# Kernel optimization log

Hardware: AMD Instinct MI355X
Metric: run time of the kernel (lower is better)

## Reference

```python
import jax, jax.numpy as jnp
import numpy as np
import math

B, S, HID, NH = 2, 2048, 1024, 16
HD = HID // NH  # head_dim = 64
TEMPERATURE = 1.0


def setup_inputs() -> dict:
    key = jax.random.key(0)
    ks = jax.random.split(key, 6)
    w = lambda k: (jax.random.normal(k, (HID, HID), dtype=jnp.float32) * 0.02)
    return {
        "hidden_states": jax.random.normal(ks[0], (B, S, HID), dtype=jnp.float32),
        "attention_mask": jnp.ones((B, S), dtype=jnp.float32),
        "Wq": w(ks[1]), "bq": jnp.zeros((HID,), jnp.float32),
        "Wk": w(ks[2]), "bk": jnp.zeros((HID,), jnp.float32),
        "Wv": w(ks[3]), "bv": jnp.zeros((HID,), jnp.float32),
        "Wo": w(ks[4]), "bo": jnp.zeros((HID,), jnp.float32),
    }


def reference(hidden_states, attention_mask, Wq, bq, Wk, bk, Wv, bv, Wo, bo):
    b, s, hid = hidden_states.shape
    heads = lambda x: x.reshape(b, s, NH, HD).transpose(0, 2, 1, 3)  # [b,h,s,d]

    q = heads(hidden_states @ Wq.T + bq)
    k = heads(hidden_states @ Wk.T + bk)
    v = heads(hidden_states @ Wv.T + bv)

    # padding mask applied multiplicatively to k and v
    m = attention_mask[:, None, :, None]  # [b,1,s,1]
    k = k * m
    v = v * m

    # auxiliary Hopfield state: k^T @ v per head -> [b,h,d,d]
    state = jnp.einsum("bhsd,bhse->bhde", k, v)

    # energy / scores
    energy = jnp.einsum("bhqd,bhkd->bhqk", q, k) / (TEMPERATURE * math.sqrt(HD))
    causal = jnp.triu(jnp.ones((s, s), dtype=bool), k=1)  # True above diagonal
    energy = jnp.where(causal[None, None], -jnp.inf, energy)
    energy = jnp.where(attention_mask[:, None, None, :] == 0, -jnp.inf, energy)

    attn = jax.nn.softmax(energy, axis=-1)
    out = jnp.einsum("bhqk,bhkd->bhqd", attn, v)
    out = out.transpose(0, 2, 1, 3).reshape(b, s, hid)
    out = out @ Wo.T + bo
    return out, state
```

## Files before the change

### kernel.cpp

```cpp
#include <hip/hip_runtime.h>
#include <hip/hip_bf16.h>

#define B_ 2
#define S_ 2048
#define HID_ 1024
#define NH_ 16
#define HD_ 64
#define MTOK (B_*S_)
#define LDQKV 3072

typedef __attribute__((ext_vector_type(8))) __bf16 bf16x8;
typedef __attribute__((ext_vector_type(4))) __bf16 bf16x4;
typedef __attribute__((ext_vector_type(4))) float f32x4;

__device__ __forceinline__ void gl16(__bf16* lds, const __bf16* g) {
  __builtin_amdgcn_global_load_lds(
      (const __attribute__((address_space(1))) void*)g,
      (__attribute__((address_space(3))) void*)lds, 16, 0, 0);
}

__global__ __launch_bounds__(256) void cast_all(
    const float* __restrict__ X,
    const float* __restrict__ Wq, const float* __restrict__ Wk,
    const float* __restrict__ Wv, const float* __restrict__ Wo,
    __bf16* __restrict__ Xb, __bf16* __restrict__ Wqkvb, __bf16* __restrict__ Wob)
{
  int i = blockIdx.x * 256 + threadIdx.x;
  const float* src; __bf16* dst; int j;
  if (i < (1 << 20))              { src = X;  dst = Xb;                 j = i; }
  else if (i < (1<<20)+(1<<18))   { src = Wq; dst = Wqkvb;              j = i - (1<<20); }
  else if (i < (1<<20)+(2<<18))   { src = Wk; dst = Wqkvb + (1<<20);    j = i - (1<<20) - (1<<18); }
  else if (i < (1<<20)+(3<<18))   { src = Wv; dst = Wqkvb + (2<<20);    j = i - (1<<20) - (2<<18); }
  else                            { src = Wo; dst = Wob;                j = i - (1<<20) - (3<<18); }
  float4 v = reinterpret_cast<const float4*>(src)[j];
  bf16x4 o;
  o[0] = (__bf16)v.x; o[1] = (__bf16)v.y; o[2] = (__bf16)v.z; o[3] = (__bf16)v.w;
  reinterpret_cast<bf16x4*>(dst)[j] = o;
}

__global__ __launch_bounds__(256) void gemm_qkv(
    const __bf16* __restrict__ A, const __bf16* __restrict__ W,
    const float* __restrict__ bq, const float* __restrict__ bk,
    const float* __restrict__ bv, const float* __restrict__ mask,
    __bf16* __restrict__ C)
{
  __shared__ __bf16 As[2][128 * 32];
  __shared__ __bf16 Bs[2][128 * 32];
  const int t = threadIdx.x;
  const int m0 = blockIdx.y * 128;
  const int n0 = blockIdx.x * 128;
  const int lane = t & 63;
  const int w = t >> 6;
  const int wr = (w >> 1) * 64;
  const int wc = (w & 1) * 64;
  const int fr = lane & 15;
  const int kg = lane >> 4;

  f32x4 acc[4][4];
  #pragma unroll
  for (int i = 0; i < 4; i++)
    #pragma unroll
    for (int j = 0; j < 4; j++) acc[i][j] = (f32x4)0.f;

  const int srow = w * 16 + (lane >> 2);
  const int scol = (lane & 3) * 8;
  const __bf16* ap0 = A + (size_t)(m0 + srow) * HID_ + scol;
  const __bf16* ap1 = A + (size_t)(m0 + 64 + srow) * HID_ + scol;
  const __bf16* wp0 = W + (size_t)(n0 + srow) * HID_ + scol;
  const __bf16* wp1 = W + (size_t)(n0 + 64 + srow) * HID_ + scol;

  #define GSTAGE(buf, koff) \
    gl16(&As[buf][w * 512], ap0 + (koff)); \
    gl16(&As[buf][2048 + w * 512], ap1 + (koff)); \
    gl16(&Bs[buf][w * 512], wp0 + (koff)); \
    gl16(&Bs[buf][2048 + w * 512], wp1 + (koff));

  GSTAGE(0, 0);
  for (int k0 = 0; k0 < HID_; k0 += 32) {
    const int cur = (k0 >> 5) & 1;
    if (k0 + 32 < HID_) {
      GSTAGE(cur ^ 1, k0 + 32);
      asm volatile("s_waitcnt vmcnt(4)" ::: "memory");
    } else {
      asm volatile("s_waitcnt vmcnt(0)" ::: "memory");
    }
    __builtin_amdgcn_sched_barrier(0);
    __builtin_amdgcn_s_barrier();
    bf16x8 af[4], bf[4];
    #pragma unroll
    for (int m = 0; m < 4; m++) af[m] = *(const bf16x8*)&As[cur][(wr + m*16 + fr) * 32 + kg*8];
    #pragma unroll
    for (int n = 0; n < 4; n++) bf[n] = *(const bf16x8*)&Bs[cur][(wc + n*16 + fr) * 32 + kg*8];
    #pragma unroll
    for (int m = 0; m < 4; m++)
      #pragma unroll
      for (int n = 0; n < 4; n++)
        acc[m][n] = __builtin_amdgcn_mfma_f32_16x16x32_bf16(af[m], bf[n], acc[m][n], 0, 0, 0);
    __builtin_amdgcn_s_barrier();
  }

  const int region = n0 >> 10;
  const float* bias = region == 0 ? bq : (region == 1 ? bk : bv);
  const int nloc = n0 & 1023;

  #pragma unroll
  for (int m = 0; m < 4; m++) {
    #pragma unroll
    for (int r = 0; r < 4; r++) {
      int row = m0 + wr + m*16 + kg*4 + r;
      float rs = region ? mask[row] : 1.f;
      #pragma unroll
      for (int n = 0; n < 4; n++) {
        int c = wc + n*16 + fr;
        float v = (acc[m][n][r] + bias[nloc + c]) * rs;
        C[(size_t)row * LDQKV + n0 + c] = (__bf16)v;
      }
    }
  }
}

__global__ __launch_bounds__(256) void gemm_o(
    const __bf16* __restrict__ A, const __bf16* __restrict__ W,
    const float* __restrict__ bias, float* __restrict__ C)
{
  __shared__ __bf16 As[2][128 * 32];
  __shared__ __bf16 Bs[2][128 * 32];
  const int t = threadIdx.x;
  const int m0 = blockIdx.y * 128;
  const int n0 = blockIdx.x * 128;
  const int lane = t & 63;
  const int w = t >> 6;
  const int wr = (w >> 1) * 64;
  const int wc = (w & 1) * 64;
  const int fr = lane & 15;
  const int kg = lane >> 4;

  f32x4 acc[4][4];
  #pragma unroll
  for (int i = 0; i < 4; i++)
    #pragma unroll
    for (int j = 0; j < 4; j++) acc[i][j] = (f32x4)0.f;

  const int srow = w * 16 + (lane >> 2);
  const int scol = (lane & 3) * 8;
  const __bf16* ap0 = A + (size_t)(m0 + srow) * HID_ + scol;
  const __bf16* ap1 = A + (size_t)(m0 + 64 + srow) * HID_ + scol;
  const __bf16* wp0 = W + (size_t)(n0 + srow) * HID_ + scol;
  const __bf16* wp1 = W + (size_t)(n0 + 64 + srow) * HID_ + scol;

  GSTAGE(0, 0);
  for (int k0 = 0; k0 < HID_; k0 += 32) {
    const int cur = (k0 >> 5) & 1;
    if (k0 + 32 < HID_) {
      GSTAGE(cur ^ 1, k0 + 32);
      asm volatile("s_waitcnt vmcnt(4)" ::: "memory");
    } else {
      asm volatile("s_waitcnt vmcnt(0)" ::: "memory");
    }
    __builtin_amdgcn_sched_barrier(0);
    __builtin_amdgcn_s_barrier();
    bf16x8 af[4], bf[4];
    #pragma unroll
    for (int m = 0; m < 4; m++) af[m] = *(const bf16x8*)&As[cur][(wr + m*16 + fr) * 32 + kg*8];
    #pragma unroll
    for (int n = 0; n < 4; n++) bf[n] = *(const bf16x8*)&Bs[cur][(wc + n*16 + fr) * 32 + kg*8];
    #pragma unroll
    for (int m = 0; m < 4; m++)
      #pragma unroll
      for (int n = 0; n < 4; n++)
        acc[m][n] = __builtin_amdgcn_mfma_f32_16x16x32_bf16(af[m], bf[n], acc[m][n], 0, 0, 0);
    __builtin_amdgcn_s_barrier();
  }

  #pragma unroll
  for (int m = 0; m < 4; m++) {
    #pragma unroll
    for (int r = 0; r < 4; r++) {
      int row = m0 + wr + m*16 + kg*4 + r;
      #pragma unroll
      for (int n = 0; n < 4; n++) {
        int col = n0 + wc + n*16 + fr;
        C[(size_t)row * HID_ + col] = acc[m][n][r] + bias[col];
      }
    }
  }
}

__global__ __launch_bounds__(256) void transpose_kv(
    const __bf16* __restrict__ Kin, const __bf16* __restrict__ Vin,
    __bf16* __restrict__ Kt, __bf16* __restrict__ Vt)
{
  __shared__ __bf16 tile[64][68];
  const int tok0 = blockIdx.x * 64;
  const int f0 = blockIdx.y * 64;
  const __bf16* in = blockIdx.z ? Vin : Kin;
  __bf16* out = blockIdx.z ? Vt : Kt;
  const int t = threadIdx.x;
  const int r = t >> 2;
  const int c0 = (t & 3) * 16;
  const __bf16* src = in + (size_t)(tok0 + r) * LDQKV + f0 + c0;
  *(bf16x8*)&tile[r][c0]     = *(const bf16x8*)src;
  *(bf16x8*)&tile[r][c0 + 8] = *(const bf16x8*)(src + 8);
  __syncthreads();
  bf16x8 o0, o1;
  #pragma unroll
  for (int j = 0; j < 8; j++) { o0[j] = tile[c0 + j][r]; o1[j] = tile[c0 + 8 + j][r]; }
  __bf16* dst = out + (size_t)(f0 + r) * MTOK + tok0 + c0;
  *(bf16x8*)dst = o0;
  *(bf16x8*)(dst + 8) = o1;
}

#define SCALE_LOG2E 0.18033688011112043f

__device__ __forceinline__ bf16x8 ld_swz(const __bf16* base, int row, int xb) {
  return *(const bf16x8*)((const char*)base + row * 128 + (xb ^ ((row & 7) << 4)));
}
__device__ __forceinline__ void st_swz16(__bf16* base, int row, int colbyte, __bf16 v) {
  *(__bf16*)((char*)base + row * 128 + (colbyte ^ ((row & 7) << 4))) = v;
}
__device__ __forceinline__ bf16x8 ld_swz256(const __bf16* base, int row, int xb) {
  return *(const bf16x8*)((const char*)base + row * 256 + (xb ^ ((row & 7) << 4)));
}

__device__ __forceinline__ void attn_tile(
    const __bf16* __restrict__ ks, const __bf16* __restrict__ vs,
    const bool (&okm)[4], __bf16* __restrict__ pw,
    const bf16x8 (&qa)[2], f32x4 (&acc)[4], f32x4& accl,
    const bf16x8 ones, int q0w, int kt, int fc, int kg)
{
  f32x4 s[4];
  #pragma unroll
  for (int n = 0; n < 4; n++) s[n] = (f32x4)0.f;
  #pragma unroll
  for (int kd = 0; kd < 2; kd++)
    #pragma unroll
    for (int n = 0; n < 4; n++) {
      bf16x8 kf = ld_swz(ks, n * 16 + fc, kd * 64 + kg * 16);
      s[n] = __builtin_amdgcn_mfma_f32_16x16x32_bf16(qa[kd], kf, s[n], 0, 0, 0);
    }

  const int g4 = kg * 4;
  const bool fullt = (kt * 64 + 63 <= q0w);
  if (fullt) {
    #pragma unroll
    for (int r = 0; r < 4; r++)
      #pragma unroll
      for (int n = 0; n < 4; n++) {
        float p = okm[n] ? __builtin_amdgcn_exp2f(s[n][r] * SCALE_LOG2E) : 0.f;
        st_swz16(pw, g4 + r, (n * 16 + fc) * 2, (__bf16)p);
      }
  } else {
    #pragma unroll
    for (int r = 0; r < 4; r++) {
      const int qg = q0w + g4 + r;
      #pragma unroll
      for (int n = 0; n < 4; n++) {
        bool ok = okm[n] && (kt * 64 + n * 16 + fc <= qg);
        float p = ok ? __builtin_amdgcn_exp2f(s[n][r] * SCALE_LOG2E) : 0.f;
        st_swz16(pw, g4 + r, (n * 16 + fc) * 2, (__bf16)p);
      }
    }
  }

  #pragma unroll
  for (int kc = 0; kc < 2; kc++) {
    bf16x8 pf = ld_swz(pw, fc, kc * 64 + kg * 16);
    accl = __builtin_amdgcn_mfma_f32_16x16x32_bf16(pf, ones, accl, 0, 0, 0);
    #pragma unroll
    for (int n = 0; n < 4; n++) {
      bf16x8 vf = ld_swz(vs, n * 16 + fc, kc * 64 + kg * 16);
      acc[n] = __builtin_amdgcn_mfma_f32_16x16x32_bf16(pf, vf, acc[n], 0, 0, 0);
    }
  }
}

__global__ __launch_bounds__(256) void flash_mfma(
    const __bf16* __restrict__ Q, const __bf16* __restrict__ K,
    const __bf16* __restrict__ Vt, const float* __restrict__ mask,
    __bf16* __restrict__ O)
{
  __shared__ __bf16 Ks[2][64 * 64];
  __shared__ __bf16 Vs[2][64 * 64];
  __shared__ __bf16 Ps[4][16 * 64];

  const int bh = blockIdx.x;
  const int qt = 31 - (int)blockIdx.y;
  const int b = bh >> 4, h = bh & 15;
  const int t = threadIdx.x;
  const int w = t >> 6;
  const int lane = t & 63;
  const int fc = lane & 15;
  const int kg = lane >> 4;
  const int g4 = kg * 4;

  const int q0w = qt * 64 + w * 16;
  const size_t tokbase = (size_t)b * S_;

  const int rr = lane >> 3;
  const int cswz = ((lane & 7) ^ rr) * 8;
  const int ktmax = qt;

  bf16x8 qa[2];
  {
    const __bf16* qp = Q + (tokbase + q0w + fc) * LDQKV + h * HD_;
    qa[0] = *(const bf16x8*)(qp + kg * 8);
    qa[1] = *(const bf16x8*)(qp + 32 + kg * 8);
  }

  const float* mp = mask + tokbase + fc;
  float mnxt[4];
  #pragma unroll
  for (int n = 0; n < 4; n++) mnxt[n] = mp[n * 16];

  const __bf16* kp0 = K + (tokbase + (size_t)(w * 16 + rr)) * LDQKV + h * HD_ + cswz;
  const __bf16* kp1 = kp0 + (size_t)8 * LDQKV;
  const __bf16* vp0 = Vt + (size_t)(h * HD_ + w * 16 + rr) * MTOK + tokbase + cswz;
  const __bf16* vp1 = vp0 + (size_t)8 * MTOK;

  gl16(&Ks[0][(w * 16) * 64],     kp0);
  gl16(&Ks[0][(w * 16 + 8) * 64], kp1);
  gl16(&Vs[0][(w * 16) * 64],     vp0);
  gl16(&Vs[0][(w * 16 + 8) * 64], vp1);
  kp0 += (size_t)64 * LDQKV; kp1 += (size_t)64 * LDQKV;
  vp0 += 64; vp1 += 64;

  bf16x8 ones;
  #pragma unroll
  for (int j = 0; j < 8; j++) ones[j] = (__bf16)1.f;

  f32x4 acc[4], accl;
  #pragma unroll
  for (int n = 0; n < 4; n++) acc[n] = (f32x4)0.f;
  accl = (f32x4)0.f;

  __bf16* pw = &Ps[w][0];

  for (int kt = 0; kt <= ktmax; ++kt) {
    const int cur = kt & 1;
    float mcur[4];
    #pragma unroll
    for (int n = 0; n < 4; n++) mcur[n] = mnxt[n];

    if (kt < ktmax) {
      #pragma unroll
      for (int n = 0; n < 4; n++) mnxt[n] = mp[(kt + 1) * 64 + n * 16];
      const int nxt = cur ^ 1;
      gl16(&Ks[nxt][(w * 16) * 64],     kp0);
      gl16(&Ks[nxt][(w * 16 + 8) * 64], kp1);
      gl16(&Vs[nxt][(w * 16) * 64],     vp0);
      gl16(&Vs[nxt][(w * 16 + 8) * 64], vp1);
      kp0 += (size_t)64 * LDQKV; kp1 += (size_t)64 * LDQKV;
      vp0 += 64; vp1 += 64;
      asm volatile("s_waitcnt vmcnt(8)" ::: "memory");
    } else {
      asm volatile("s_waitcnt vmcnt(0)" ::: "memory");
    }
    __builtin_amdgcn_sched_barrier(0);
    __builtin_amdgcn_s_barrier();

    bool okm[4];
    #pragma unroll
    for (int n = 0; n < 4; n++) okm[n] = (mcur[n] != 0.f);

    attn_tile(&Ks[cur][0], &Vs[cur][0], okm, pw, qa, acc, accl, ones, q0w, kt, fc, kg);

    __builtin_amdgcn_s_barrier();
  }

  #pragma unroll
  for (int r = 0; r < 4; r++) {
    float inv = accl[r] > 0.f ? 1.f / accl[r] : 0.f;
    __bf16* op = O + (tokbase + q0w + g4 + r) * HID_ + h * HD_;
    #pragma unroll
    for (int n = 0; n < 4; n++)
      op[n * 16 + fc] = (__bf16)(acc[n][r] * inv);
  }
}

__global__ __launch_bounds__(256) void state_mfma(
    const __bf16* __restrict__ Kt, const __bf16* __restrict__ Vt,
    float* __restrict__ part)
{
  __shared__ __bf16 Kl[64 * 128];
  __shared__ __bf16 Vl[64 * 128];
  const int bh = blockIdx.x, sc = blockIdx.y;
  const int b = bh >> 4, h = bh & 15;
  const int t = threadIdx.x;
  const int w = t >> 6;
  const int lane = t & 63;
  const int fc = lane & 15;
  const int kg = lane >> 4;
  const size_t colbase = (size_t)b * S_ + sc * 128;
  const int rloc = lane >> 4;
  const int cb = (lane & 15) * 16;

  #pragma unroll
  for (int c = 0; c < 4; c++) {
    int row = w * 16 + c * 4 + rloc;
    int scol = (cb ^ ((row & 7) << 4)) >> 1;
    gl16(&Kl[(w * 16 + c * 4) * 128], Kt + (size_t)(h * HD_ + row) * MTOK + colbase + scol);
    gl16(&Vl[(w * 16 + c * 4) * 128], Vt + (size_t)(h * HD_ + row) * MTOK + colbase + scol);
  }
  __syncthreads();

  f32x4 acc[4];
  #pragma unroll
  for (int n = 0; n < 4; n++) acc[n] = (f32x4)0.f;
  #pragma unroll
  for (int ks = 0; ks < 4; ks++) {
    bf16x8 af = ld_swz256(Kl, w * 16 + fc, ks * 64 + kg * 16);
    #pragma unroll
    for (int n = 0; n < 4; n++) {
      bf16x8 bfr = ld_swz256(Vl, n * 16 + fc, ks * 64 + kg * 16);
      acc[n] = __builtin_amdgcn_mfma_f32_16x16x32_bf16(af, bfr, acc[n], 0, 0, 0);
    }
  }

  float* dst = part + (((size_t)bh * 16 + sc) << 12);
  #pragma unroll
  for (int n = 0; n < 4; n++)
    #pragma unroll
    for (int r = 0; r < 4; r++)
      dst[(w * 16 + kg * 4 + r) * 64 + n * 16 + fc] = acc[n][r];
}

__global__ __launch_bounds__(256) void state_reduce(
    const float* __restrict__ part, float* __restrict__ out)
{
  int i = blockIdx.x * 256 + threadIdx.x;
  int bh = i >> 12, de = i & 4095;
  float s = 0.f;
  #pragma unroll
  for (int sc = 0; sc < 16; sc++) s += part[(((size_t)bh * 16 + sc) << 12) + de];
  out[i] = s;
}

extern "C" void kernel_launch(void* const* d_in, const int* in_sizes, int n_in,
                              void* d_out, int out_size, void* d_ws, size_t ws_size,
                              hipStream_t stream)
{
  const float* hs   = (const float*)d_in[0];
  const float* mask = (const float*)d_in[1];
  const float* Wq   = (const float*)d_in[2];
  const float* bq   = (const float*)d_in[3];
  const float* Wk   = (const float*)d_in[4];
  const float* bk   = (const float*)d_in[5];
  const float* Wv   = (const float*)d_in[6];
  const float* bv   = (const float*)d_in[7];
  const float* Wo   = (const float*)d_in[8];
  const float* bo   = (const float*)d_in[9];
  float* out = (float*)d_out;

  char* ws = (char*)d_ws;
  __bf16* Wqkvb = (__bf16*)(ws);
  __bf16* Wob   = (__bf16*)(ws + (6u  << 20));
  __bf16* Xb    = (__bf16*)(ws + (8u  << 20));
  __bf16* QKV   = (__bf16*)(ws + (16u << 20));
  __bf16* Ob    = (__bf16*)(ws + (40u << 20));
  __bf16* Ktg   = (__bf16*)(ws + (48u << 20));

  cast_all<<<8192, 256, 0, stream>>>(hs, Wq, Wk, Wv, Wo, Xb, Wqkvb, Wob);

  gemm_qkv<<<dim3(LDQKV / 128, MTOK / 128), 256, 0, stream>>>(
      Xb, Wqkvb, bq, bk, bv, mask, QKV);

  __bf16* Vtg = Xb;
  transpose_kv<<<dim3(MTOK / 64, HID_ / 64, 2), 256, 0, stream>>>(
      QKV + 1024, QKV + 2048, Ktg, Vtg);

  flash_mfma<<<dim3(B_ * NH_, 32), 256, 0, stream>>>(
      QKV, QKV + 1024, Vtg, mask, Ob);

  gemm_o<<<dim3(HID_ / 128, MTOK / 128), 256, 0, stream>>>(Ob, Wob, bo, out);

  float* part = (float*)Ob;
  state_mfma<<<dim3(B_ * NH_, 16), 256, 0, stream>>>(Ktg, Vtg, part);
  state_reduce<<<512, 256, 0, stream>>>(part, out + (size_t)MTOK * HID_);
}
```

Baseline: 136.0 us.

## Triple-buffer GEMM pipeline with swizzled LDS, fuse state reduce into gemm_o

After: 126.3 us. -7.1%, faster.

```diff
diff --git a/kernel.cpp b/kernel.cpp
--- a/kernel.cpp
+++ b/kernel.cpp
@@ -18,6 +18,8 @@
       (const __attribute__((address_space(1))) void*)g,
       (__attribute__((address_space(3))) void*)lds, 16, 0, 0);
 }
+
+__device__ __forceinline__ int gswz(int row) { return ((row ^ (row >> 2)) & 3) << 4; }
 
 __global__ __launch_bounds__(256) void cast_all(
     const float* __restrict__ X,
@@ -44,8 +46,7 @@
     const float* __restrict__ bv, const float* __restrict__ mask,
     __bf16* __restrict__ C)
 {
-  __shared__ __bf16 As[2][128 * 32];
-  __shared__ __bf16 Bs[2][128 * 32];
+  __shared__ __bf16 SM[24576];
   const int t = threadIdx.x;
   const int m0 = blockIdx.y * 128;
   const int n0 = blockIdx.x * 128;
@@ -63,40 +64,51 @@
     for (int j = 0; j < 4; j++) acc[i][j] = (f32x4)0.f;
 
   const int srow = w * 16 + (lane >> 2);
-  const int scol = (lane & 3) * 8;
-  const __bf16* ap0 = A + (size_t)(m0 + srow) * HID_ + scol;
-  const __bf16* ap1 = A + (size_t)(m0 + 64 + srow) * HID_ + scol;
-  const __bf16* wp0 = W + (size_t)(n0 + srow) * HID_ + scol;
-  const __bf16* wp1 = W + (size_t)(n0 + 64 + srow) * HID_ + scol;
-
-  #define GSTAGE(buf, koff) \
-    gl16(&As[buf][w * 512], ap0 + (koff)); \
-    gl16(&As[buf][2048 + w * 512], ap1 + (koff)); \
-    gl16(&Bs[buf][w * 512], wp0 + (koff)); \
-    gl16(&Bs[buf][2048 + w * 512], wp1 + (koff));
-
-  GSTAGE(0, 0);
-  for (int k0 = 0; k0 < HID_; k0 += 32) {
-    const int cur = (k0 >> 5) & 1;
-    if (k0 + 32 < HID_) {
-      GSTAGE(cur ^ 1, k0 + 32);
-      asm volatile("s_waitcnt vmcnt(4)" ::: "memory");
-    } else {
-      asm volatile("s_waitcnt vmcnt(0)" ::: "memory");
-    }
+  const int scolb = ((lane & 3) * 16) ^ gswz(srow);
+  const __bf16* ap0 = A + (size_t)(m0 + srow) * HID_ + (scolb >> 1);
+  const __bf16* ap1 = A + (size_t)(m0 + 64 + srow) * HID_ + (scolb >> 1);
+  const __bf16* wp0 = W + (size_t)(n0 + srow) * HID_ + (scolb >> 1);
+  const __bf16* wp1 = W + (size_t)(n0 + 64 + srow) * HID_ + (scolb >> 1);
+
+  #define STAGE3(buf, koff) { \
+    __bf16* ab = SM + (buf) * 4096; \
+    __bf16* bb = SM + 12288 + (buf) * 4096; \
+    gl16(ab + w * 512, ap0 + (koff)); \
+    gl16(ab + 2048 + w * 512, ap1 + (koff)); \
+    gl16(bb + w * 512, wp0 + (koff)); \
+    gl16(bb + 2048 + w * 512, wp1 + (koff)); }
+
+  STAGE3(0, 0);
+  STAGE3(1, 32);
+  int bc = 0, bp2 = 2;
+  for (int step = 0; step < 32; ++step) {
+    if (step + 1 < 32) { asm volatile("s_waitcnt vmcnt(4)" ::: "memory"); }
+    else               { asm volatile("s_waitcnt vmcnt(0)" ::: "memory"); }
     __builtin_amdgcn_sched_barrier(0);
     __builtin_amdgcn_s_barrier();
+    if (step + 2 < 32) STAGE3(bp2, (step + 2) * 32);
+
+    const __bf16* ab = SM + bc * 4096;
+    const __bf16* bb = SM + 12288 + bc * 4096;
     bf16x8 af[4], bf[4];
     #pragma unroll
-    for (int m = 0; m < 4; m++) af[m] = *(const bf16x8*)&As[cur][(wr + m*16 + fr) * 32 + kg*8];
-    #pragma unroll
-    for (int n = 0; n < 4; n++) bf[n] = *(const bf16x8*)&Bs[cur][(wc + n*16 + fr) * 32 + kg*8];
+    for (int m = 0; m < 4; m++) {
+      int row = wr + m*16 + fr;
+      af[m] = *(const bf16x8*)((const char*)ab + row * 64 + ((kg * 16) ^ gswz(row)));
+    }
+    #pragma unroll
+    for (int n = 0; n < 4; n++) {
+      int row = wc + n*16 + fr;
+      bf[n] = *(const bf16x8*)((const char*)bb + row * 64 + ((kg * 16) ^ gswz(row)));
+    }
     #pragma unroll
     for (int m = 0; m < 4; m++)
       #pragma unroll
       for (int n = 0; n < 4; n++)
         acc[m][n] = __builtin_amdgcn_mfma_f32_16x16x32_bf16(af[m], bf[n], acc[m][n], 0, 0, 0);
-    __builtin_amdgcn_s_barrier();
+
+    bc = (bc == 2) ? 0 : bc + 1;
+    bp2 = (bp2 == 2) ? 0 : bp2 + 1;
   }
 
   const int region = n0 >> 10;
@@ -112,75 +124,7 @@
       #pragma unroll
       for (int n = 0; n < 4; n++) {
         int c = wc + n*16 + fr;
-        float v = (acc[m][n][r] + bias[nloc + c]) * rs;
-        C[(size_t)row * LDQKV + n0 + c] = (__bf16)v;
-      }
-    }
-  }
-}
-
-__global__ __launch_bounds__(256) void gemm_o(
-    const __bf16* __restrict__ A, const __bf16* __restrict__ W,
-    const float* __restrict__ bias, float* __restrict__ C)
-{
-  __shared__ __bf16 As[2][128 * 32];
-  __shared__ __bf16 Bs[2][128 * 32];
-  const int t = threadIdx.x;
-  const int m0 = blockIdx.y * 128;
-  const int n0 = blockIdx.x * 128;
-  const int lane = t & 63;
-  const int w = t >> 6;
-  const int wr = (w >> 1) * 64;
-  const int wc = (w & 1) * 64;
-  const int fr = lane & 15;
-  const int kg = lane >> 4;
-
-  f32x4 acc[4][4];
-  #pragma unroll
-  for (int i = 0; i < 4; i++)
-    #pragma unroll
-    for (int j = 0; j < 4; j++) acc[i][j] = (f32x4)0.f;
-
-  const int srow = w * 16 + (lane >> 2);
-  const int scol = (lane & 3) * 8;
-  const __bf16* ap0 = A + (size_t)(m0 + srow) * HID_ + scol;
-  const __bf16* ap1 = A + (size_t)(m0 + 64 + srow) * HID_ + scol;
-  const __bf16* wp0 = W + (size_t)(n0 + srow) * HID_ + scol;
-  const __bf16* wp1 = W + (size_t)(n0 + 64 + srow) * HID_ + scol;
-
-  GSTAGE(0, 0);
-  for (int k0 = 0; k0 < HID_; k0 += 32) {
-    const int cur = (k0 >> 5) & 1;
-    if (k0 + 32 < HID_) {
-      GSTAGE(cur ^ 1, k0 + 32);
-      asm volatile("s_waitcnt vmcnt(4)" ::: "memory");
-    } else {
-      asm volatile("s_waitcnt vmcnt(0)" ::: "memory");
-    }
-    __builtin_amdgcn_sched_barrier(0);
-    __builtin_amdgcn_s_barrier();
-    bf16x8 af[4], bf[4];
-    #pragma unroll
-    for (int m = 0; m < 4; m++) af[m] = *(const bf16x8*)&As[cur][(wr + m*16 + fr) * 32 + kg*8];
-    #pragma unroll
-    for (int n = 0; n < 4; n++) bf[n] = *(const bf16x8*)&Bs[cur][(wc + n*16 + fr) * 32 + kg*8];
-    #pragma unroll
-    for (int m = 0; m < 4; m++)
-      #pragma unroll
-      for (int n = 0; n < 4; n++)
-        acc[m][n] = __builtin_amdgcn_mfma_f32_16x16x32_bf16(af[m], bf[n], acc[m][n], 0, 0, 0);
-    __builtin_amdgcn_s_barrier();
-  }
-
-  #pragma unroll
-  for (int m = 0; m < 4; m++) {
-    #pragma unroll
-    for (int r = 0; r < 4; r++) {
-      int row = m0 + wr + m*16 + kg*4 + r;
-      #pragma unroll
-      for (int n = 0; n < 4; n++) {
-        int col = n0 + wc + n*16 + fr;
-        C[(size_t)row * HID_ + col] = acc[m][n][r] + bias[col];
+        C[(size_t)row * LDQKV + n0 + c] = (__bf16)((acc[m][n][r] + bias[nloc + c]) * rs);
       }
     }
   }
@@ -210,6 +154,98 @@
   *(bf16x8*)(dst + 8) = o1;
 }
 
+__global__ __launch_bounds__(256) void gemm_o(
+    const __bf16* __restrict__ A, const __bf16* __restrict__ W,
+    const float* __restrict__ bias, const float* __restrict__ part,
+    float* __restrict__ C)
+{
+  if (blockIdx.y >= 32) {
+    const int bl = blockIdx.x + (blockIdx.y - 32) * 8;
+    const int tid = bl * 256 + threadIdx.x;
+    float* outState = C + (size_t)MTOK * HID_;
+    #pragma unroll 4
+    for (int e = 0; e < 32; e++) {
+      int i = e * 4096 + tid;
+      int bh = i >> 12, de = i & 4095;
+      float s = 0.f;
+      #pragma unroll
+      for (int sc = 0; sc < 8; sc++) s += part[(size_t)((bh << 3) + sc) * 4096 + de];
+      outState[i] = s;
+    }
+    return;
+  }
+
+  __shared__ __bf16 SM[24576];
+  const int t = threadIdx.x;
+  const int m0 = blockIdx.y * 128;
+  const int n0 = blockIdx.x * 128;
+  const int lane = t & 63;
+  const int w = t >> 6;
+  const int wr = (w >> 1) * 64;
+  const int wc = (w & 1) * 64;
+  const int fr = lane & 15;
+  const int kg = lane >> 4;
+
+  f32x4 acc[4][4];
+  #pragma unroll
+  for (int i = 0; i < 4; i++)
+    #pragma unroll
+    for (int j = 0; j < 4; j++) acc[i][j] = (f32x4)0.f;
+
+  const int srow = w * 16 + (lane >> 2);
+  const int scolb = ((lane & 3) * 16) ^ gswz(srow);
+  const __bf16* ap0 = A + (size_t)(m0 + srow) * HID_ + (scolb >> 1);
+  const __bf16* ap1 = A + (size_t)(m0 + 64 + srow) * HID_ + (scolb >> 1);
+  const __bf16* wp0 = W + (size_t)(n0 + srow) * HID_ + (scolb >> 1);
+  const __bf16* wp1 = W + (size_t)(n0 + 64 + srow) * HID_ + (scolb >> 1);
+
+  STAGE3(0, 0);
+  STAGE3(1, 32);
+  int bc = 0, bp2 = 2;
+  for (int step = 0; step < 32; ++step) {
+    if (step + 1 < 32) { asm volatile("s_waitcnt vmcnt(4)" ::: "memory"); }
+    else               { asm volatile("s_waitcnt vmcnt(0)" ::: "memory"); }
+    __builtin_amdgcn_sched_barrier(0);
+    __builtin_amdgcn_s_barrier();
+    if (step + 2 < 32) STAGE3(bp2, (step + 2) * 32);
+
+    const __bf16* ab = SM + bc * 4096;
+    const __bf16* bb = SM + 12288 + bc * 4096;
+    bf16x8 af[4], bf[4];
+    #pragma unroll
+    for (int m = 0; m < 4; m++) {
+      int row = wr + m*16 + fr;
+      af[m] = *(const bf16x8*)((const char*)ab + row * 64 + ((kg * 16) ^ gswz(row)));
+    }
+    #pragma unroll
+    for (int n = 0; n < 4; n++) {
+      int row = wc + n*16 + fr;
+      bf[n] = *(const bf16x8*)((const char*)bb + row * 64 + ((kg * 16) ^ gswz(row)));
+    }
+    #pragma unroll
+    for (int m = 0; m < 4; m++)
+      #pragma unroll
+      for (int n = 0; n < 4; n++)
+        acc[m][n] = __builtin_amdgcn_mfma_f32_16x16x32_bf16(af[m], bf[n], acc[m][n], 0, 0, 0);
+
+    bc = (bc == 2) ? 0 : bc + 1;
+    bp2 = (bp2 == 2) ? 0 : bp2 + 1;
+  }
+
+  #pragma unroll
+  for (int m = 0; m < 4; m++) {
+    #pragma unroll
+    for (int r = 0; r < 4; r++) {
+      int row = m0 + wr + m*16 + kg*4 + r;
+      #pragma unroll
+      for (int n = 0; n < 4; n++) {
+        int col = n0 + wc + n*16 + fr;
+        C[(size_t)row * HID_ + col] = acc[m][n][r] + bias[col];
+      }
+    }
+  }
+}
+
 #define SCALE_LOG2E 0.18033688011112043f
 
 __device__ __forceinline__ bf16x8 ld_swz(const __bf16* base, int row, int xb) {
@@ -231,6 +267,7 @@
   f32x4 s[4];
   #pragma unroll
   for (int n = 0; n < 4; n++) s[n] = (f32x4)0.f;
+  __builtin_amdgcn_s_setprio(1);
   #pragma unroll
   for (int kd = 0; kd < 2; kd++)
     #pragma unroll
@@ -238,6 +275,7 @@
       bf16x8 kf = ld_swz(ks, n * 16 + fc, kd * 64 + kg * 16);
       s[n] = __builtin_amdgcn_mfma_f32_16x16x32_bf16(qa[kd], kf, s[n], 0, 0, 0);
     }
+  __builtin_amdgcn_s_setprio(0);
 
   const int g4 = kg * 4;
   const bool fullt = (kt * 64 + 63 <= q0w);
@@ -262,6 +300,7 @@
     }
   }
 
+  __builtin_amdgcn_s_setprio(1);
   #pragma unroll
   for (int kc = 0; kc < 2; kc++) {
     bf16x8 pf = ld_swz(pw, fc, kc * 64 + kg * 16);
@@ -272,6 +311,7 @@
       acc[n] = __builtin_amdgcn_mfma_f32_16x16x32_bf16(pf, vf, acc[n], 0, 0, 0);
     }
   }
+  __builtin_amdgcn_s_setprio(0);
 }
 
 __global__ __launch_bounds__(256) void flash_mfma(
@@ -390,49 +430,42 @@
   const int lane = t & 63;
   const int fc = lane & 15;
   const int kg = lane >> 4;
-  const size_t colbase = (size_t)b * S_ + sc * 128;
   const int rloc = lane >> 4;
   const int cb = (lane & 15) * 16;
 
-  #pragma unroll
-  for (int c = 0; c < 4; c++) {
-    int row = w * 16 + c * 4 + rloc;
-    int scol = (cb ^ ((row & 7) << 4)) >> 1;
-    gl16(&Kl[(w * 16 + c * 4) * 128], Kt + (size_t)(h * HD_ + row) * MTOK + colbase + scol);
-    gl16(&Vl[(w * 16 + c * 4) * 128], Vt + (size_t)(h * HD_ + row) * MTOK + colbase + scol);
-  }
-  __syncthreads();
-
   f32x4 acc[4];
   #pragma unroll
   for (int n = 0; n < 4; n++) acc[n] = (f32x4)0.f;
-  #pragma unroll
-  for (int ks = 0; ks < 4; ks++) {
-    bf16x8 af = ld_swz256(Kl, w * 16 + fc, ks * 64 + kg * 16);
-    #pragma unroll
-    for (int n = 0; n < 4; n++) {
-      bf16x8 bfr = ld_swz256(Vl, n * 16 + fc, ks * 64 + kg * 16);
-      acc[n] = __builtin_amdgcn_mfma_f32_16x16x32_bf16(af, bfr, acc[n], 0, 0, 0);
-    }
-  }
-
-  float* dst = part + (((size_t)bh * 16 + sc) << 12);
+
+  for (int ch = 0; ch < 2; ch++) {
+    const size_t colbase = (size_t)b * S_ + sc * 256 + ch * 128;
+    __syncthreads();
+    #pragma unroll
+    for (int c = 0; c < 4; c++) {
+      int row = w * 16 + c * 4 + rloc;
+      int scol = (cb ^ ((row & 7) << 4)) >> 1;
+      gl16(&Kl[(w * 16 + c * 4) * 128], Kt + (size_t)(h * HD_ + row) * MTOK + colbase + scol);
+      gl16(&Vl[(w * 16 + c * 4) * 128], Vt + (size_t)(h * HD_ + row) * MTOK + colbase + scol);
+    }
+    __syncthreads();
+
+    #pragma unroll
+    for (int ks = 0; ks < 4; ks++) {
+      bf16x8 af = ld_swz256(Kl, w * 16 + fc, ks * 64 + kg * 16);
+      #pragma unroll
+      for (int n = 0; n < 4; n++) {
+        bf16x8 bfr = ld_swz256(Vl, n * 16 + fc, ks * 64 + kg * 16);
+        acc[n] = __builtin_amdgcn_mfma_f32_16x16x32_bf16(af, bfr, acc[n], 0, 0, 0);
+      }
+    }
+  }
+
+  float* dst = part + ((size_t)((bh << 3) + sc) << 12);
   #pragma unroll
   for (int n = 0; n < 4; n++)
     #pragma unroll
     for (int r = 0; r < 4; r++)
       dst[(w * 16 + kg * 4 + r) * 64 + n * 16 + fc] = acc[n][r];
-}
-
-__global__ __launch_bounds__(256) void state_reduce(
-    const float* __restrict__ part, float* __restrict__ out)
-{
-  int i = blockIdx.x * 256 + threadIdx.x;
-  int bh = i >> 12, de = i & 4095;
-  float s = 0.f;
-  #pragma unroll
-  for (int sc = 0; sc < 16; sc++) s += part[(((size_t)bh * 16 + sc) << 12) + de];
-  out[i] = s;
 }
 
 extern "C" void kernel_launch(void* const* d_in, const int* in_sizes, int n_in,
@@ -471,9 +504,8 @@
   flash_mfma<<<dim3(B_ * NH_, 32), 256, 0, stream>>>(
       QKV, QKV + 1024, Vtg, mask, Ob);
 
-  gemm_o<<<dim3(HID_ / 128, MTOK / 128), 256, 0, stream>>>(Ob, Wob, bo, out);
-
-  float* part = (float*)Ob;
-  state_mfma<<<dim3(B_ * NH_, 16), 256, 0, stream>>>(Ktg, Vtg, part);
-  state_reduce<<<512, 256, 0, stream>>>(part, out + (size_t)MTOK * HID_);
-}
+  float* part = (float*)Wqkvb;
+  state_mfma<<<dim3(B_ * NH_, 8), 256, 0, stream>>>(Ktg, Vtg, part);
+
+  gemm_o<<<dim3(HID_ / 128, 34), 256, 0, stream>>>(Ob, Wob, bo, part, out);
+}
```
